# Optimization experiments

Measured on AMD Instinct MI355X. Metric: run time of the kernel, lower is better.

Reference implementation:

```python
import jax, jax.numpy as jnp
import numpy as np

D_MODEL = 1024
NUM_HEADS = 16
D_INTERNAL = D_MODEL // NUM_HEADS
ROPE_BASE = 10000.0


def justnorm(x):
    return x / jnp.linalg.norm(x, axis=-1, keepdims=True)


def rotate_half(x):
    h = x.shape[-1] // 2
    return jnp.concatenate([-x[..., h:], x[..., :h]], axis=-1)


def setup_inputs() -> dict:
    key = jax.random.key(0)
    ks = jax.random.split(key, 8)
    B, T, dm, H, di = 4, 2048, D_MODEL, NUM_HEADS, D_INTERNAL
    x = jax.random.normal(ks[0], (B, T, dm), dtype=jnp.float32)
    stdev_h = 1.0 / (dm + di) ** 0.5
    qkv = jax.random.uniform(ks[1], (H, 3 * di, dm), minval=-stdev_h, maxval=stdev_h, dtype=jnp.float32)
    qkv = justnorm(qkv)  # per-row L2 normalization as in torch init
    sqk = (dm ** -0.5) * jnp.ones((H, di), dtype=jnp.float32)
    stdev = 1.0 / (4 * dm + dm) ** 0.5
    W_O = justnorm(jax.random.uniform(ks[2], (dm, dm), minval=-stdev, maxval=stdev, dtype=jnp.float32))
    Wu = justnorm(jax.random.uniform(ks[3], (8 * dm, dm), minval=-stdev, maxval=stdev, dtype=jnp.float32))
    Wv = justnorm(jax.random.uniform(ks[4], (dm, 4 * dm), minval=-stdev, maxval=stdev, dtype=jnp.float32))
    attn_alpha = (dm ** -0.5) * jnp.ones((dm,), dtype=jnp.float32)
    mlp_alpha = jnp.ones((dm,), dtype=jnp.float32)
    suv = jnp.ones((8 * dm,), dtype=jnp.float32)
    return {"x": x, "qkv": qkv, "sqk": sqk, "W_O": W_O, "Wu": Wu, "Wv": Wv,
            "attn_alpha": attn_alpha, "mlp_alpha": mlp_alpha, "suv": suv}


def _forward(x, qkv, sqk, W_O, Wu, Wv, attn_alpha, mlp_alpha, suv):
    B, T, dm = x.shape
    H = qkv.shape[0]
    di = qkv.shape[1] // 3
    sqrt_dm = jnp.sqrt(jnp.asarray(dm, x.dtype))
    # Per-head QKV projection, batched over heads: [B,H,T,3*di]
    qkv_out = jnp.einsum('btd,hed->bhte', x, qkv)
    Q, K, V = jnp.split(qkv_out, 3, axis=-1)
    # RoPE over full d_internal
    inv_freq = 1.0 / (ROPE_BASE ** (jnp.arange(0, di, 2, dtype=jnp.float32) / di))
    freqs = jnp.arange(T, dtype=jnp.float32)[:, None] * inv_freq[None, :]
    emb = jnp.concatenate([freqs, freqs], axis=-1)  # [T, di]
    cos, sin = jnp.cos(emb), jnp.sin(emb)
    Q = Q * cos + rotate_half(Q) * sin
    K = K * cos + rotate_half(K) * sin
    # sqk effective scale: sqk * (1.0 / d_model**-0.5)
    sqk_eff = sqk * sqrt_dm  # [H, di]
    Q = justnorm(Q) * sqk_eff[None, :, None, :]
    K = justnorm(K) * sqk_eff[None, :, None, :]
    # SDPA with non-standard scale = d_model**0.5, causal (eval mode)
    scores = jnp.einsum('bhqd,bhkd->bhqk', Q, K) * sqrt_dm
    causal = jnp.tril(jnp.ones((T, T), dtype=bool))
    scores = jnp.where(causal[None, None], scores, jnp.finfo(x.dtype).min)
    attn = jax.nn.softmax(scores, axis=-1)
    out = jnp.einsum('bhqk,bhkd->bhqd', attn, V)
    t = out.transpose(0, 2, 1, 3).reshape(B, T, dm)
    t = t @ W_O.T
    # nGPT-style attention lerp residual: attn_alpha * (0.05 / d_model**-0.5)
    lr = jnp.abs(attn_alpha * (0.05 * sqrt_dm))
    A = justnorm(x)
    Bn = justnorm(t)
    x1 = justnorm(A + lr * (Bn - A))
    # SwiGLU MLP
    uv = x1 @ Wu.T
    uv = (suv * sqrt_dm) * uv
    tn = justnorm(uv)
    u, v = jnp.split(tn, 2, axis=-1)
    res = u * jax.nn.silu(v)
    t = res @ Wv.T
    lr2 = jnp.abs(mlp_alpha * 0.05)
    A = justnorm(x1)
    Bn = justnorm(t)
    return justnorm(A + lr2 * (Bn - A))


def reference(x, qkv, sqk, W_O, Wu, Wv, attn_alpha, mlp_alpha, suv):
    return _forward(x, qkv, sqk, W_O, Wu, Wv, attn_alpha, mlp_alpha, suv)
```

## Files before the change

### kernel.cpp

```cpp
#include <hip/hip_runtime.h>
#include <hip/hip_bf16.h>


#define B_   4
#define T_   2048
#define DM   1024
#define H_   16
#define DI   64
#define NROW (B_ * T_)

using bf16 = __hip_bfloat16;
typedef __attribute__((ext_vector_type(8))) short bfrag;
typedef __attribute__((ext_vector_type(4))) float f4;

#define EXPB 46.166241f

__device__ __forceinline__ float ldf(const float* p) { return *p; }
__device__ __forceinline__ float ldf(const bf16* p)  { return __bfloat162float(*p); }
__device__ __forceinline__ void  stf(float* p, float v) { *p = v; }
__device__ __forceinline__ void  stf(bf16* p, float v)  { *p = __float2bfloat16(v); }

__device__ __forceinline__ unsigned short bfbits(float a) {
    bf16 h = __float2bfloat16(a);
    return __builtin_bit_cast(unsigned short, h);
}
__device__ __forceinline__ unsigned pk2(float a, float b) {
    return (unsigned)bfbits(a) | ((unsigned)bfbits(b) << 16);
}
__device__ __forceinline__ unsigned pk2t(float a, float b) {
    return __builtin_amdgcn_perm(__builtin_bit_cast(unsigned, b),
                                 __builtin_bit_cast(unsigned, a), 0x07060302u);
}

__device__ __forceinline__ float fexp2(float x) {
    return __builtin_amdgcn_exp2f(x);
}

__device__ __forceinline__ float wave_sum(float v) {
#pragma unroll
    for (int off = 32; off; off >>= 1) v += __shfl_xor(v, off, 64);
    return v;
}

__device__ __forceinline__ float block_sum(float v) {
    __shared__ float sm[4];
    int lane = threadIdx.x & 63, w = threadIdx.x >> 6;
    v = wave_sum(v);
    __syncthreads();
    if (lane == 0) sm[w] = v;
    __syncthreads();
    return sm[0] + sm[1] + sm[2] + sm[3];
}

typedef __attribute__((address_space(1))) const void g_void;
typedef __attribute__((address_space(3))) void l_void;
__device__ __forceinline__ void gl_lds(const void* g, void* l) {
    __builtin_amdgcn_global_load_lds((g_void*)g, (l_void*)l, 16, 0, 0);
}

__global__ __launch_bounds__(256)
void f32_to_bf16_k(const float* __restrict__ in, bf16* __restrict__ out, long n)
{
    long i = ((long)blockIdx.x * 256 + threadIdx.x) * 8;
    if (i >= n) return;
    float4 a = *(const float4*)(in + i);
    float4 b = *(const float4*)(in + i + 4);
    union { bfrag f; unsigned u[4]; } o;
    o.u[0] = pk2(a.x, a.y); o.u[1] = pk2(a.z, a.w);
    o.u[2] = pk2(b.x, b.y); o.u[3] = pk2(b.z, b.w);
    *(bfrag*)(out + i) = o.f;
}

template <typename TC>
__global__ __launch_bounds__(256)
void gemm_bf16(const bf16* __restrict__ A, const bf16* __restrict__ Bm,
               TC* __restrict__ C, int M, int N, int K)
{
    __shared__ bf16 lds[2][2][128 * 32];
    const int tid  = threadIdx.x;
    const int w    = tid >> 6, lane = tid & 63;
    const int g    = lane >> 4, c = lane & 15;
    const int m0   = blockIdx.y * 128, n0 = blockIdx.x * 128;
    const int wm   = w >> 1, wn = w & 1;

    const int srow = (lane >> 2);
    const int skc  = 8 * (lane & 3);

    f4 acc[4][4] = {{{0,0,0,0}}};

    const int NT = K >> 5;

#pragma unroll
    for (int q = 0; q < 2; q++) {
        int cidx = w * 2 + q;
        int row  = 16 * cidx + srow;
        gl_lds(A + (long)(m0 + row) * K + skc, &lds[0][0][cidx * 512]);
        gl_lds(Bm + (long)(n0 + row) * K + skc, &lds[0][1][cidx * 512]);
    }
    __syncthreads();

    for (int t = 0; t < NT; t++) {
        int cur = t & 1;
        if (t + 1 < NT) {
            int k0 = (t + 1) << 5;
#pragma unroll
            for (int q = 0; q < 2; q++) {
                int cidx = w * 2 + q;
                int row  = 16 * cidx + srow;
                gl_lds(A + (long)(m0 + row) * K + k0 + skc, &lds[cur ^ 1][0][cidx * 512]);
                gl_lds(Bm + (long)(n0 + row) * K + k0 + skc, &lds[cur ^ 1][1][cidx * 512]);
            }
        }
        const bf16* bufA = &lds[cur][0][0];
        const bf16* bufB = &lds[cur][1][0];
        bfrag af[4], bb[4];
#pragma unroll
        for (int mi = 0; mi < 4; mi++)
            af[mi] = *(const bfrag*)(bufA + (64 * wm + 16 * mi + c) * 32 + 8 * g);
#pragma unroll
        for (int ni = 0; ni < 4; ni++)
            bb[ni] = *(const bfrag*)(bufB + (64 * wn + 16 * ni + c) * 32 + 8 * g);
#pragma unroll
        for (int mi = 0; mi < 4; mi++)
#pragma unroll
            for (int ni = 0; ni < 4; ni++)
                acc[mi][ni] = __builtin_amdgcn_mfma_f32_16x16x32_bf16(
                    af[mi], bb[ni], acc[mi][ni], 0, 0, 0);
        __syncthreads();
    }

#pragma unroll
    for (int mi = 0; mi < 4; mi++)
#pragma unroll
        for (int ni = 0; ni < 4; ni++) {
            long row = m0 + 64 * wm + 16 * mi + 4 * g;
            long col = n0 + 64 * wn + 16 * ni + c;
#pragma unroll
            for (int r = 0; r < 4; r++)
                stf(&C[(row + r) * N + col], acc[mi][ni][r]);
        }
}

template <typename TC>
__global__ __launch_bounds__(512, 2)
void gemm_bf16_256(const bf16* __restrict__ A, const bf16* __restrict__ Bm,
                   TC* __restrict__ C, int M, int N, int K)
{
    __shared__ bf16 lds[2][2][256 * 64];
    const int tid  = threadIdx.x;
    const int w    = tid >> 6, lane = tid & 63;
    const int g    = lane >> 4, c = lane & 15;
    const int m0   = blockIdx.y * 256, n0 = blockIdx.x * 256;
    const int wm   = w & 1, wn = w >> 1;
    const int srow8 = lane >> 3;
    const int swz   = 8 * ((lane & 7) ^ srow8);
    const int cx    = c & 7;

    f4 acc[8][4] = {{{0,0,0,0}}};

    const int NT = K >> 6;

    auto STAGE = [&](int buf, int t) {
        int k0 = t << 6;
#pragma unroll
        for (int i = 0; i < 4; i++) {
            int rb = w * 32 + i * 8;
            gl_lds(A  + (long)(m0 + rb + srow8) * K + k0 + swz, &lds[buf][0][rb * 64]);
            gl_lds(Bm + (long)(n0 + rb + srow8) * K + k0 + swz, &lds[buf][1][rb * 64]);
        }
    };

    STAGE(0, 0);
    STAGE(1, 1);
    asm volatile("s_waitcnt vmcnt(8)" ::: "memory");
    __builtin_amdgcn_s_barrier();

    for (int t = 0; t < NT; t++) {
        const bf16* bufA = &lds[t & 1][0][0];
        const bf16* bufB = &lds[t & 1][1][0];

        bfrag a0[4][2], b0[4][2];
#pragma unroll
        for (int mi = 0; mi < 4; mi++)
#pragma unroll
            for (int kk = 0; kk < 2; kk++)
                a0[mi][kk] = *(const bfrag*)(bufA + (wm * 128 + mi * 16 + c) * 64
                                                  + 8 * ((4 * kk + g) ^ cx));
#pragma unroll
        for (int ni = 0; ni < 4; ni++)
#pragma unroll
            for (int kk = 0; kk < 2; kk++)
                b0[ni][kk] = *(const bfrag*)(bufB + (wn * 64 + ni * 16 + c) * 64
                                                  + 8 * ((4 * kk + g) ^ cx));
        asm volatile("s_waitcnt lgkmcnt(0)" ::: "memory");
        __builtin_amdgcn_sched_barrier(0);
        __builtin_amdgcn_s_setprio(1);
#pragma unroll
        for (int mi = 0; mi < 4; mi++)
#pragma unroll
            for (int ni = 0; ni < 4; ni++) {
                acc[mi][ni] = __builtin_amdgcn_mfma_f32_16x16x32_bf16(
                    a0[mi][0], b0[ni][0], acc[mi][ni], 0, 0, 0);
                acc[mi][ni] = __builtin_amdgcn_mfma_f32_16x16x32_bf16(
                    a0[mi][1], b0[ni][1], acc[mi][ni], 0, 0, 0);
            }
        __builtin_amdgcn_s_setprio(0);

        bfrag a1[4][2];
#pragma unroll
        for (int mi = 0; mi < 4; mi++)
#pragma unroll
            for (int kk = 0; kk < 2; kk++)
                a1[mi][kk] = *(const bfrag*)(bufA + (wm * 128 + (mi + 4) * 16 + c) * 64
                                                  + 8 * ((4 * kk + g) ^ cx));
        asm volatile("s_waitcnt lgkmcnt(0)" ::: "memory");
        __builtin_amdgcn_sched_barrier(0);
        __builtin_amdgcn_s_setprio(1);
#pragma unroll
        for (int mi = 0; mi < 4; mi++)
#pragma unroll
            for (int ni = 0; ni < 4; ni++) {
                acc[mi + 4][ni] = __builtin_amdgcn_mfma_f32_16x16x32_bf16(
                    a1[mi][0], b0[ni][0], acc[mi + 4][ni], 0, 0, 0);
                acc[mi + 4][ni] = __builtin_amdgcn_mfma_f32_16x16x32_bf16(
                    a1[mi][1], b0[ni][1], acc[mi + 4][ni], 0, 0, 0);
            }
        __builtin_amdgcn_s_setprio(0);

        __builtin_amdgcn_s_barrier();
        if (t + 2 < NT) {
            STAGE(t & 1, t + 2);
            asm volatile("s_waitcnt vmcnt(8)" ::: "memory");
        } else if (t + 1 < NT) {
            asm volatile("s_waitcnt vmcnt(0)" ::: "memory");
        }
        __builtin_amdgcn_s_barrier();
    }

#pragma unroll
    for (int mi = 0; mi < 8; mi++)
#pragma unroll
        for (int ni = 0; ni < 4; ni++) {
            long row = m0 + wm * 128 + mi * 16 + 4 * g;
            long col = n0 + wn * 64 + ni * 16 + c;
#pragma unroll
            for (int r = 0; r < 4; r++)
                stf(&C[(row + r) * N + col], acc[mi][ni][r]);
        }
}

__global__ __launch_bounds__(256)
void rope_norm_qk(const bf16* __restrict__ QKVb, const float* __restrict__ sqk,
                  bf16* __restrict__ Qb, bf16* __restrict__ Kb, bf16* __restrict__ Vt)
{
    int gw   = (blockIdx.x * 256 + threadIdx.x) >> 6;
    int lane = threadIdx.x & 63;
    int h = gw / NROW, row = gw % NROW, t = row % T_, b = row / T_;

    const bf16* base = QKVb + (long)row * 3072 + h * 192;
    float q = __bfloat162float(base[lane]);
    float k = __bfloat162float(base[64 + lane]);
    bf16  v = base[128 + lane];

    int   j   = lane & 31;
    float inv = expf(-(float)j * (9.210340371976184f / 32.f));
    float ang = (float)t * inv;
    float s = sinf(ang), cc = cosf(ang);

    float qp = __shfl_xor(q, 32, 64);
    float kp = __shfl_xor(k, 32, 64);
    float sgn = (lane < 32) ? -1.f : 1.f;
    float qr = q * cc + sgn * qp * s;
    float kr = k * cc + sgn * kp * s;

    float qs = wave_sum(qr * qr);
    float ks = wave_sum(kr * kr);
    float se = sqk[h * 64 + lane] * 32.f;

    long idx = ((long)h * NROW + row) * 64 + lane;
    Qb[idx] = __float2bfloat16(qr * rsqrtf(qs) * se * EXPB);
    Kb[idx] = __float2bfloat16(kr * rsqrtf(ks) * se);
    Vt[((long)(h * B_ + b) * 64 + lane) * T_ + t] = v;
}

__global__ __launch_bounds__(256)
void attn_mfma(const bf16* __restrict__ Qb, const bf16* __restrict__ Kb,
               const bf16* __restrict__ Vt, bf16* __restrict__ O)
{
    __shared__ bf16 kv[2][2][64 * 64];

    int orig   = blockIdx.x;
    int xcd    = orig & 7;
    int rest   = orig >> 3;
    int bh     = xcd * 8 + (rest & 7);
    int blkraw = rest >> 3;
    int blk    = (blkraw & 1) ? (15 - (blkraw >> 1)) : (blkraw >> 1);
    int w      = threadIdx.x >> 6;
    int pr     = blk * 4 + w;
    int h = bh >> 2, b = bh & 3;

    int lane = threadIdx.x & 63;
    int g = lane >> 4, c = lane & 15;

    const bf16* kbase = Kb + ((long)h * NROW + (long)b * T_) * 64;
    const bf16* vbase = Vt + (long)(h * B_ + b) * 64 * (long)T_;

    int q0A = pr * 16, q0B = (127 - pr) * 16;
    const bf16* qbA = Qb + ((long)h * NROW + (long)b * T_ + q0A) * 64;
    const bf16* qbB = Qb + ((long)h * NROW + (long)b * T_ + q0B) * 64;
    bfrag qfA0 = *(const bfrag*)(qbA + (long)c * 64 + 8 * g);
    bfrag qfA1 = *(const bfrag*)(qbA + (long)c * 64 + 32 + 8 * g);
    bfrag qfB0 = *(const bfrag*)(qbB + (long)c * 64 + 8 * g);
    bfrag qfB1 = *(const bfrag*)(qbB + (long)c * 64 + 32 + 8 * g);

    const f4 CINIT = {-EXPB, -EXPB, -EXPB, -EXPB};

    f4 otA[4] = {{0,0,0,0},{0,0,0,0},{0,0,0,0},{0,0,0,0}};
    f4 otB[4] = {{0,0,0,0},{0,0,0,0},{0,0,0,0},{0,0,0,0}};
    float lA = 0.f, lB = 0.f;

    const int nA = blk, nB = 31 - blk, KT = nB;
    int qgA = q0A + c, qgB = q0B + c;

    const int srow8  = lane >> 3;
    const int swz    = 8 * ((lane & 7) ^ srow8);

    auto STAGE = [&](int buf, int kt) {
        int k0 = kt * 64;
#pragma unroll
        for (int i = 0; i < 2; i++) {
            int rb  = (w * 2 + i) * 8;
            int row = rb + srow8;
            gl_lds(kbase + (long)(k0 + row) * 64 + swz, &kv[buf][0][rb * 64]);
            gl_lds(vbase + (long)row * T_ + k0 + swz,   &kv[buf][1][rb * 64]);
        }
    };

    STAGE(0, 0);
    __syncthreads();

    const int cx = c & 7;

    for (int kt = 0; kt <= KT; kt++) {
        int buf = kt & 1;
        if (kt < KT) STAGE(buf ^ 1, kt + 1);

        const bf16* Kl = &kv[buf][0][0];
        const bf16* Vl = &kv[buf][1][0];
        int k0 = kt * 64;
        bool actA = (kt <= nA);
        unsigned wvA[8], wvB[8];

#pragma unroll
        for (int kb = 0; kb < 4; kb++) {
            const bf16* kr = Kl + (16 * kb + c) * 64;
            bfrag ka = *(const bfrag*)(kr + 8 * (g ^ cx));
            bfrag kc = *(const bfrag*)(kr + 8 * ((g | 4) ^ cx));

            f4 sB = __builtin_amdgcn_mfma_f32_16x16x32_bf16(ka, qfB0, CINIT, 0, 0, 0);
            sB = __builtin_amdgcn_mfma_f32_16x16x32_bf16(kc, qfB1, sB, 0, 0, 0);
            if (kt == nB) {
#pragma unroll
                for (int r = 0; r < 4; r++)
                    if (k0 + 16 * kb + 4 * g + r > qgB) sB[r] = -1e30f;
            }
            float eB0 = fexp2(sB[0]), eB1 = fexp2(sB[1]);
            float eB2 = fexp2(sB[2]), eB3 = fexp2(sB[3]);
            lB += (eB0 + eB1) + (eB2 + eB3);
            wvB[2 * kb]     = pk2t(eB0, eB1);
            wvB[2 * kb + 1] = pk2t(eB2, eB3);

            if (actA) {
                f4 sA = __builtin_amdgcn_mfma_f32_16x16x32_bf16(ka, qfA0, CINIT, 0, 0, 0);
                sA = __builtin_amdgcn_mfma_f32_16x16x32_bf16(kc, qfA1, sA, 0, 0, 0);
                if (kt == nA) {
#pragma unroll
                    for (int r = 0; r < 4; r++)
                        if (k0 + 16 * kb + 4 * g + r > qgA) sA[r] = -1e30f;
                }
                float eA0 = fexp2(sA[0]), eA1 = fexp2(sA[1]);
                float eA2 = fexp2(sA[2]), eA3 = fexp2(sA[3]);
                lA += (eA0 + eA1) + (eA2 + eA3);
                wvA[2 * kb]     = pk2t(eA0, eA1);
                wvA[2 * kb + 1] = pk2t(eA2, eA3);
            }
        }

#pragma unroll
        for (int p = 0; p < 2; p++) {
            int s0l = c + 32 * (g & 1), s1l = s0l + 16;
            bool hi = (g >= 2);

            unsigned Bb0 = (unsigned)__shfl((int)wvB[4 * p + 0], s0l, 64);
            unsigned Bb1 = (unsigned)__shfl((int)wvB[4 * p + 1], s0l, 64);
            unsigned Bb2 = (unsigned)__shfl((int)wvB[4 * p + 2], s0l, 64);
            unsigned Bb3 = (unsigned)__shfl((int)wvB[4 * p + 3], s0l, 64);
            unsigned Bb4 = (unsigned)__shfl((int)wvB[4 * p + 0], s1l, 64);
            unsigned Bb5 = (unsigned)__shfl((int)wvB[4 * p + 1], s1l, 64);
            unsigned Bb6 = (unsigned)__shfl((int)wvB[4 * p + 2], s1l, 64);
            unsigned Bb7 = (unsigned)__shfl((int)wvB[4 * p + 3], s1l, 64);
            union { bfrag f; unsigned u[4]; } pfB;
            pfB.u[0] = hi ? Bb2 : Bb0;
            pfB.u[1] = hi ? Bb3 : Bb1;
            pfB.u[2] = hi ? Bb6 : Bb4;
            pfB.u[3] = hi ? Bb7 : Bb5;

            union { bfrag f; unsigned u[4]; } pfA;
            if (actA) {
                unsigned Ab0 = (unsigned)__shfl((int)wvA[4 * p + 0], s0l, 64);
                unsigned Ab1 = (unsigned)__shfl((int)wvA[4 * p + 1], s0l, 64);
                unsigned Ab2 = (unsigned)__shfl((int)wvA[4 * p + 2], s0l, 64);
                unsigned Ab3 = (unsigned)__shfl((int)wvA[4 * p + 3], s0l, 64);
                unsigned Ab4 = (unsigned)__shfl((int)wvA[4 * p + 0], s1l, 64);
                unsigned Ab5 = (unsigned)__shfl((int)wvA[4 * p + 1], s1l, 64);
                unsigned Ab6 = (unsigned)__shfl((int)wvA[4 * p + 2], s1l, 64);
                unsigned Ab7 = (unsigned)__shfl((int)wvA[4 * p + 3], s1l, 64);
                pfA.u[0] = hi ? Ab2 : Ab0;
                pfA.u[1] = hi ? Ab3 : Ab1;
                pfA.u[2] = hi ? Ab6 : Ab4;
                pfA.u[3] = hi ? Ab7 : Ab5;
            }

#pragma unroll
            for (int dblk = 0; dblk < 4; dblk++) {
                bfrag vf = *(const bfrag*)(Vl + (16 * dblk + c) * 64
                                              + 8 * (((p << 2) | g) ^ cx));
                otB[dblk] = __builtin_amdgcn_mfma_f32_16x16x32_bf16(vf, pfB.f, otB[dblk], 0, 0, 0);
                if (actA)
                    otA[dblk] = __builtin_amdgcn_mfma_f32_16x16x32_bf16(vf, pfA.f, otA[dblk], 0, 0, 0);
            }
        }
        __syncthreads();
    }

    lA += __shfl_xor(lA, 16, 64); lA += __shfl_xor(lA, 32, 64);
    lB += __shfl_xor(lB, 16, 64); lB += __shfl_xor(lB, 32, 64);

    float invA = 1.f / lA, invB = 1.f / lB;
    long orowA = (long)(b * T_ + q0A + c) * DM + h * 64;
    long orowB = (long)(b * T_ + q0B + c) * DM + h * 64;
#pragma unroll
    for (int dblk = 0; dblk < 4; dblk++)
#pragma unroll
        for (int r = 0; r < 4; r++) {
            O[orowA + 16 * dblk + 4 * g + r] = __float2bfloat16(otA[dblk][r] * invA);
            O[orowB + 16 * dblk + 4 * g + r] = __float2bfloat16(otB[dblk][r] * invB);
        }
}

template <typename TX, typename TT>
__global__ __launch_bounds__(256)
void lerp_norm(const TX* __restrict__ X, const TT* __restrict__ Tt,
               const float* __restrict__ alpha, float ascale,
               float* __restrict__ OutF, bf16* __restrict__ OutB)
{
    long row = blockIdx.x;
    const TX* xr = X  + row * DM;
    const TT* tr = Tt + row * DM;
    int tid = threadIdx.x;

    float xs[4], ts[4], sx = 0.f, st = 0.f;
#pragma unroll
    for (int i = 0; i < 4; i++) {
        int d = tid + 256 * i;
        xs[i] = ldf(&xr[d]); ts[i] = ldf(&tr[d]);
        sx += xs[i] * xs[i]; st += ts[i] * ts[i];
    }
    sx = block_sum(sx);
    st = block_sum(st);
    float ix = rsqrtf(sx), it = rsqrtf(st);

    float ys[4], sy = 0.f;
#pragma unroll
    for (int i = 0; i < 4; i++) {
        int d = tid + 256 * i;
        float a  = xs[i] * ix;
        float bn = ts[i] * it;
        float lr = fabsf(alpha[d] * ascale);
        ys[i] = a + lr * (bn - a);
        sy += ys[i] * ys[i];
    }
    sy = block_sum(sy);
    float iy = rsqrtf(sy);
#pragma unroll
    for (int i = 0; i < 4; i++) {
        int d = tid + 256 * i;
        float o = ys[i] * iy;
        if (OutF) OutF[row * DM + d] = o;
        if (OutB) OutB[row * DM + d] = __float2bfloat16(o);
    }
}

__global__ __launch_bounds__(256)
void mlp_act(const bf16* __restrict__ UV, const float* __restrict__ suv,
             bf16* __restrict__ R)
{
    long row = blockIdx.x;
    const bf16* ur = UV + row * 8192;
    int tid = threadIdx.x;

    float ss = 0.f;
#pragma unroll
    for (int i = 0; i < 32; i++) {
        int j = tid + 256 * i;
        float v = __bfloat162float(ur[j]) * suv[j] * 32.f;
        ss += v * v;
    }
    ss = block_sum(ss);
    float inv = rsqrtf(ss);

#pragma unroll
    for (int i = 0; i < 16; i++) {
        int j = tid + 256 * i;
        float u = __bfloat162float(ur[j])        * suv[j]        * 32.f * inv;
        float v = __bfloat162float(ur[4096 + j]) * suv[4096 + j] * 32.f * inv;
        float sil = v / (1.f + __expf(-v));
        R[row * 4096 + j] = __float2bfloat16(u * sil);
    }
}

extern "C" void kernel_launch(void* const* d_in, const int* in_sizes, int n_in,
                              void* d_out, int out_size, void* d_ws, size_t ws_size,
                              hipStream_t stream)
{
    const float* x          = (const float*)d_in[0];
    const float* qkv_w      = (const float*)d_in[1];
    const float* sqk        = (const float*)d_in[2];
    const float* W_O        = (const float*)d_in[3];
    const float* Wu         = (const float*)d_in[4];
    const float* Wv         = (const float*)d_in[5];
    const float* attn_alpha = (const float*)d_in[6];
    const float* mlp_alpha  = (const float*)d_in[7];
    const float* suv        = (const float*)d_in[8];
    float* out = (float*)d_out;

    const long MiB = 1048576;
    char* ws = (char*)d_ws;
    bf16*  x1b   = (bf16*) (ws + 32 * MiB);
    bf16*  QKVb  = (bf16*) (ws + 48 * MiB);
    bf16*  tbuf  = (bf16*) (ws + 48 * MiB);
    bf16*  uv    = (bf16*) (ws + 48 * MiB);
    bf16*  t2    = (bf16*) (ws + 48 * MiB);
    bf16*  xb    = (bf16*) (ws + 144 * MiB);
    bf16*  Qb    = (bf16*) (ws + 144 * MiB);
    bf16*  Wub   = (bf16*) (ws + 144 * MiB);
    bf16*  Kb    = (bf16*) (ws + 160 * MiB);
    bf16*  Vt    = (bf16*) (ws + 176 * MiB);
    bf16*  Wvb   = (bf16*) (ws + 176 * MiB);
    bf16*  res   = (bf16*) (ws + 112 * MiB);
    bf16*  qkvwb = (bf16*) (ws + 192 * MiB);
    bf16*  attno = (bf16*) (ws + 192 * MiB);
    bf16*  Wob   = (bf16*) (ws + 208 * MiB);

    f32_to_bf16_k<<<4096, 256, 0, stream>>>(x, xb, 8388608L);
    f32_to_bf16_k<<<1536, 256, 0, stream>>>(qkv_w, qkvwb, 3145728L);
    f32_to_bf16_k<<<512,  256, 0, stream>>>(W_O, Wob, 1048576L);

    gemm_bf16_256<bf16><<<dim3(12, 32), 512, 0, stream>>>(xb, qkvwb, QKVb, NROW, 3072, DM);

    rope_norm_qk<<<(H_ * NROW) / 4, 256, 0, stream>>>(QKVb, sqk, Qb, Kb, Vt);

    attn_mfma<<<1024, 256, 0, stream>>>(Qb, Kb, Vt, attno);

    gemm_bf16<bf16><<<dim3(8, 64), 256, 0, stream>>>(attno, Wob, tbuf, NROW, DM, DM);

    lerp_norm<float, bf16><<<NROW, 256, 0, stream>>>(x, tbuf, attn_alpha, 1.6f,
                                                     (float*)nullptr, x1b);

    f32_to_bf16_k<<<4096, 256, 0, stream>>>(Wu, Wub, 8388608L);
    f32_to_bf16_k<<<2048, 256, 0, stream>>>(Wv, Wvb, 4194304L);

    for (int half = 0; half < 2; half++) {
        gemm_bf16_256<bf16><<<dim3(32, 16), 512, 0, stream>>>(
            x1b + (long)half * 4096 * DM, Wub, uv, 4096, 8 * DM, DM);
        mlp_act<<<4096, 256, 0, stream>>>(uv, suv, res + (long)half * 4096 * 4096);
    }

    gemm_bf16<bf16><<<dim3(8, 64), 256, 0, stream>>>(res, Wvb, t2, NROW, DM, 4 * DM);

    lerp_norm<bf16, bf16><<<NROW, 256, 0, stream>>>(x1b, t2, mlp_alpha, 0.05f,
                                                    out, (bf16*)nullptr);
}
```

Baseline: 573.5 us.

## Split-K the down-projection GEMM with 256 tiles and sum partials in lerp_norm

The final MLP down-projection (K=4096) now runs on the 256x256 GEMM kernel, split into two K-halves along grid z. Each half writes fp32 partials to its own buffer, and the closing lerp_norm adds the two partials as it loads them. This raises the block count for a GEMM that otherwise gives only 128 large tiles, at the cost of extra fp32 partial writes and reads. RoPE also switches to hardware sin/cos on range-reduced revolutions with exp2, replacing the library expf/sinf/cosf.

```diff
diff --git a/kernel.cpp b/kernel.cpp
--- a/kernel.cpp
+++ b/kernel.cpp
@@ -144,8 +144,12 @@
 template <typename TC>
 __global__ __launch_bounds__(512, 2)
 void gemm_bf16_256(const bf16* __restrict__ A, const bf16* __restrict__ Bm,
-                   TC* __restrict__ C, int M, int N, int K)
-{
+                   TC* __restrict__ C, int M, int N, int K, int LD, long sCz)
+{
+    A  += (long)blockIdx.z * K;
+    Bm += (long)blockIdx.z * K;
+    C  += (long)blockIdx.z * sCz;
+
     __shared__ bf16 lds[2][2][256 * 64];
     const int tid  = threadIdx.x;
     const int w    = tid >> 6, lane = tid & 63;
@@ -165,8 +169,8 @@
 #pragma unroll
         for (int i = 0; i < 4; i++) {
             int rb = w * 32 + i * 8;
-            gl_lds(A  + (long)(m0 + rb + srow8) * K + k0 + swz, &lds[buf][0][rb * 64]);
-            gl_lds(Bm + (long)(n0 + rb + srow8) * K + k0 + swz, &lds[buf][1][rb * 64]);
+            gl_lds(A  + (long)(m0 + rb + srow8) * LD + k0 + swz, &lds[buf][0][rb * 64]);
+            gl_lds(Bm + (long)(n0 + rb + srow8) * LD + k0 + swz, &lds[buf][1][rb * 64]);
         }
     };
 
@@ -263,9 +267,11 @@
     bf16  v = base[128 + lane];
 
     int   j   = lane & 31;
-    float inv = expf(-(float)j * (9.210340371976184f / 32.f));
-    float ang = (float)t * inv;
-    float s = sinf(ang), cc = cosf(ang);
+    float inv_rev = fexp2(-(float)j * 0.41524101f) * 0.15915494f;
+    float ar = (float)t * inv_rev;
+    ar = ar - floorf(ar);
+    float s  = __builtin_amdgcn_sinf(ar);
+    float cc = __builtin_amdgcn_cosf(ar);
 
     float qp = __shfl_xor(q, 32, 64);
     float kp = __shfl_xor(k, 32, 64);
@@ -451,19 +457,22 @@
 template <typename TX, typename TT>
 __global__ __launch_bounds__(256)
 void lerp_norm(const TX* __restrict__ X, const TT* __restrict__ Tt,
-               const float* __restrict__ alpha, float ascale,
-               float* __restrict__ OutF, bf16* __restrict__ OutB)
+               const TT* __restrict__ Tt2, const float* __restrict__ alpha,
+               float ascale, float* __restrict__ OutF, bf16* __restrict__ OutB)
 {
     long row = blockIdx.x;
     const TX* xr = X  + row * DM;
     const TT* tr = Tt + row * DM;
+    const TT* t2r = Tt2 ? Tt2 + row * DM : nullptr;
     int tid = threadIdx.x;
 
     float xs[4], ts[4], sx = 0.f, st = 0.f;
 #pragma unroll
     for (int i = 0; i < 4; i++) {
         int d = tid + 256 * i;
-        xs[i] = ldf(&xr[d]); ts[i] = ldf(&tr[d]);
+        xs[i] = ldf(&xr[d]);
+        ts[i] = ldf(&tr[d]);
+        if (t2r) ts[i] += ldf(&t2r[d]);
         sx += xs[i] * xs[i]; st += ts[i] * ts[i];
     }
     sx = block_sum(sx);
@@ -540,7 +549,8 @@
     bf16*  QKVb  = (bf16*) (ws + 48 * MiB);
     bf16*  tbuf  = (bf16*) (ws + 48 * MiB);
     bf16*  uv    = (bf16*) (ws + 48 * MiB);
-    bf16*  t2    = (bf16*) (ws + 48 * MiB);
+    float* t2a   = (float*)(ws + 48 * MiB);
+    float* t2b   = (float*)(ws + 80 * MiB);
     bf16*  xb    = (bf16*) (ws + 144 * MiB);
     bf16*  Qb    = (bf16*) (ws + 144 * MiB);
     bf16*  Wub   = (bf16*) (ws + 144 * MiB);
@@ -556,7 +566,8 @@
     f32_to_bf16_k<<<1536, 256, 0, stream>>>(qkv_w, qkvwb, 3145728L);
     f32_to_bf16_k<<<512,  256, 0, stream>>>(W_O, Wob, 1048576L);
 
-    gemm_bf16_256<bf16><<<dim3(12, 32), 512, 0, stream>>>(xb, qkvwb, QKVb, NROW, 3072, DM);
+    gemm_bf16_256<bf16><<<dim3(12, 32, 1), 512, 0, stream>>>(
+        xb, qkvwb, QKVb, NROW, 3072, DM, DM, 0L);
 
     rope_norm_qk<<<(H_ * NROW) / 4, 256, 0, stream>>>(QKVb, sqk, Qb, Kb, Vt);
 
@@ -564,20 +575,21 @@
 
     gemm_bf16<bf16><<<dim3(8, 64), 256, 0, stream>>>(attno, Wob, tbuf, NROW, DM, DM);
 
-    lerp_norm<float, bf16><<<NROW, 256, 0, stream>>>(x, tbuf, attn_alpha, 1.6f,
-                                                     (float*)nullptr, x1b);
+    lerp_norm<float, bf16><<<NROW, 256, 0, stream>>>(
+        x, tbuf, (const bf16*)nullptr, attn_alpha, 1.6f, (float*)nullptr, x1b);
 
     f32_to_bf16_k<<<4096, 256, 0, stream>>>(Wu, Wub, 8388608L);
     f32_to_bf16_k<<<2048, 256, 0, stream>>>(Wv, Wvb, 4194304L);
 
     for (int half = 0; half < 2; half++) {
-        gemm_bf16_256<bf16><<<dim3(32, 16), 512, 0, stream>>>(
-            x1b + (long)half * 4096 * DM, Wub, uv, 4096, 8 * DM, DM);
+        gemm_bf16_256<bf16><<<dim3(32, 16, 1), 512, 0, stream>>>(
+            x1b + (long)half * 4096 * DM, Wub, uv, 4096, 8 * DM, DM, DM, 0L);
         mlp_act<<<4096, 256, 0, stream>>>(uv, suv, res + (long)half * 4096 * 4096);
     }
 
-    gemm_bf16<bf16><<<dim3(8, 64), 256, 0, stream>>>(res, Wvb, t2, NROW, DM, 4 * DM);
-
-    lerp_norm<bf16, bf16><<<NROW, 256, 0, stream>>>(x1b, t2, mlp_alpha, 0.05f,
-                                                    out, (bf16*)nullptr);
-}
+    gemm_bf16_256<float><<<dim3(4, 32, 2), 512, 0, stream>>>(
+        res, Wvb, t2a, NROW, DM, 2048, 4 * DM, 8388608L);
+
+    lerp_norm<bf16, float><<<NROW, 256, 0, stream>>>(
+        x1b, t2a, t2b, mlp_alpha, 0.05f, out, (bf16*)nullptr);
+}
```

Measured after the change: 559.3 us. 2.5% less time.
